# Optimization experiments

Measured on AMD Instinct MI355X. Metric: run time of the kernel, lower is better.

## Reference

```python
import jax, jax.numpy as jnp
import numpy as np

H = 128            # hidden_dim
R = 16             # num_rbf
L = 3              # num_atom_encoder_layers
LAT = 32           # latent_dim
NUM_ATOM_TYPES = 64
CUTOFF = 5.0       # atom_cutoff
N_RES = 2048
DEG = 16           # avg radius-graph degree
_PATTERN = np.array([19, 20, 21, 22, 23, 24, 25, 22])  # ragged atoms/residue, mean 22


def setup_inputs() -> dict:
    key = jax.random.key(0)
    ks = jax.random.split(key, 16)
    apr = np.tile(_PATTERN, N_RES // len(_PATTERN))        # (N,) atoms per residue
    A = int(apr.sum())                                     # 45056 atoms
    E = A * DEG                                            # 720896 edges
    rng = np.random.default_rng(0)

    def gl(k, shape, fan_in):
        return jax.random.normal(k, shape, jnp.float32) * (fan_in ** -0.5)

    return {
        "atom_coords": jax.random.normal(ks[0], (A, 3), jnp.float32) * 10.0,
        "atom_types": jax.random.randint(ks[1], (A,), 0, NUM_ATOM_TYPES),
        "residue_indices": jnp.asarray(np.repeat(np.arange(N_RES), apr)),
        "residue_types": jax.random.randint(ks[2], (N_RES,), 0, 4),
        "atoms_per_residue": jnp.asarray(apr),
        "edge_src": jnp.asarray(rng.integers(0, A, E)),
        "edge_dst": jnp.asarray(rng.integers(0, A, E)),
        # learned parameters
        "atom_embed": gl(ks[3], (NUM_ATOM_TYPES, H), 1.0),
        "residue_embed": gl(ks[4], (4, H), 1.0),
        "We1": gl(ks[5], (L, 2 * H + R, H), 2 * H + R), "be1": jnp.zeros((L, H)),
        "We2": gl(ks[6], (L, H, H), H), "be2": jnp.zeros((L, H)),
        "Wh1": gl(ks[7], (L, 2 * H, H), 2 * H), "bh1": jnp.zeros((L, H)),
        "Wh2": gl(ks[8], (L, H, H), H), "bh2": jnp.zeros((L, H)),
        "Wq": gl(ks[9], (H, H), H), "bq": jnp.zeros((H,)),
        "Wk": gl(ks[10], (H, H), H), "bk": jnp.zeros((H,)),
        "Wv": gl(ks[11], (H, H), H), "bv": jnp.zeros((H,)),
        "Wmu": gl(ks[12], (H, LAT), H), "bmu": jnp.zeros((LAT,)),
        "Wlv": gl(ks[13], (H, LAT), H) * 0.01, "blv": jnp.full((LAT,), -2.0),
    }


def reference(atom_coords, atom_types, residue_indices, residue_types,
              atoms_per_residue, edge_src, edge_dst,
              atom_embed, residue_embed,
              We1, be1, We2, be2, Wh1, bh1, Wh2, bh2,
              Wq, bq, Wk, bk, Wv, bv, Wmu, bmu, Wlv, blv):
    A = atom_coords.shape[0]
    N = residue_types.shape[0]
    coords = atom_coords - atom_coords.mean(0, keepdims=True)  # center_coords

    # Gaussian radial basis expansion of edge distances
    d = jnp.linalg.norm(coords[edge_src] - coords[edge_dst], axis=-1)  # (E,)
    centers = jnp.linspace(0.0, CUTOFF, R)
    gamma = (R / CUTOFF) ** 2
    edge_attr = jnp.exp(-gamma * (d[:, None] - centers) ** 2)          # (E,R)

    # atom features: atom-type embed + residue-type embed scattered to atoms
    res_emb = residue_embed[residue_types]                             # (N,H)
    h = atom_embed[atom_types] + res_emb[residue_indices]              # (A,H)

    # EGNN layers (update_coords=False): message MLP -> sum-agg -> residual node MLP
    for l in range(L):
        m = jnp.concatenate([h[edge_src], h[edge_dst], edge_attr], axis=-1)  # (E,2H+R)
        m = jax.nn.silu(m @ We1[l] + be1[l])
        m = jax.nn.silu(m @ We2[l] + be2[l])                                  # (E,H)
        agg = jax.ops.segment_sum(m, edge_dst, num_segments=A)               # (A,H)
        u = jnp.concatenate([h, agg], axis=-1)                               # (A,2H)
        u = jax.nn.silu(u @ Wh1[l] + bh1[l])
        h = h + (u @ Wh2[l] + bh2[l])

    # segment (per-residue) attention pooling of atoms -> residues
    q = res_emb @ Wq + bq                                              # (N,H)
    k = h @ Wk + bk                                                    # (A,H)
    v = h @ Wv + bv                                                    # (A,H)
    scores = jnp.sum(q[residue_indices] * k, axis=-1) * (H ** -0.5)    # (A,)
    smax = jax.ops.segment_max(scores, residue_indices, num_segments=N)
    ex = jnp.exp(scores - smax[residue_indices])
    denom = jax.ops.segment_sum(ex, residue_indices, num_segments=N)
    w = ex / denom[residue_indices]
    pooled = jax.ops.segment_sum(w[:, None] * v, residue_indices, num_segments=N)  # (N,H)

    mu = pooled @ Wmu + bmu
    logvar = jnp.clip(pooled @ Wlv + blv, -10.0, 2.0)
    return mu, logvar
```

## Files before the change

### kernel.cpp

```cpp
#include <hip/hip_runtime.h>
#include <hip/hip_bf16.h>

#define H 128
#define LATD 32

typedef __attribute__((ext_vector_type(8))) _Float16 half8t;
typedef __attribute__((ext_vector_type(4))) _Float16 half4t;
typedef __attribute__((ext_vector_type(2))) _Float16 half2t;
typedef __attribute__((ext_vector_type(8))) unsigned short u16x8;
typedef __attribute__((ext_vector_type(4))) float f32x4;

#define OFF_RBF 0
#define OFF_W2  12288
#define OFF_PROJ 61440
#define OFF_H1  159744
#define OFF_H2  258048
#define OFF_KV  307200
#define OFF_RBF16 339968
#define WP_TOTAL 346112

__device__ __forceinline__ float silu_f(float x) {
  return x * __builtin_amdgcn_rcpf(1.0f + __expf(-x));
}
__device__ __forceinline__ unsigned short f16u(float x) {
  _Float16 hh = (_Float16)x;
  return *(unsigned short*)&hh;
}

__global__ void k_dist(const float* __restrict__ coords,
                       const int* __restrict__ esrc, const int* __restrict__ edst,
                       float* __restrict__ dbuf, int* __restrict__ cnt, int E) {
  int e = blockIdx.x * blockDim.x + threadIdx.x;
  if (e >= E) return;
  int s = esrc[e], t = edst[e];
  float dx = coords[3*s+0] - coords[3*t+0];
  float dy = coords[3*s+1] - coords[3*t+1];
  float dz = coords[3*s+2] - coords[3*t+2];
  dbuf[e] = sqrtf(dx*dx + dy*dy + dz*dz);
  atomicAdd(&cnt[t], 1);
}

__global__ __launch_bounds__(1024) void k_scanA(const int* __restrict__ cnt,
                                                int* __restrict__ cursor,
                                                int* __restrict__ bsum, int A) {
  __shared__ int buf[1024];
  int tid = threadIdx.x;
  int i = blockIdx.x * 1024 + tid;
  int v = (i < A) ? cnt[i] : 0;
  buf[tid] = v;
  __syncthreads();
  #pragma unroll
  for (int off = 1; off < 1024; off <<= 1) {
    int nv = (tid >= off) ? buf[tid - off] : 0;
    __syncthreads();
    buf[tid] += nv;
    __syncthreads();
  }
  if (i < A) cursor[i] = buf[tid] - v;
  if (tid == 1023) bsum[blockIdx.x] = buf[1023];
}

__global__ void k_scanB(int* __restrict__ bsum, int nb) {
  int lane = threadIdx.x;
  int v = (lane < nb) ? bsum[lane] : 0;
  int s = v;
  #pragma unroll
  for (int off = 1; off < 64; off <<= 1) {
    int nv = __shfl_up(s, off);
    if (lane >= off) s += nv;
  }
  if (lane < nb) bsum[lane] = s - v;
}

__global__ void k_scatter(const int* __restrict__ edst, int* __restrict__ cursor,
                          const int* __restrict__ bsum,
                          int* __restrict__ eperm, int E) {
  int e = blockIdx.x * blockDim.x + threadIdx.x;
  if (e >= E) return;
  int t = edst[e];
  int p = atomicAdd(&cursor[t], 1) + bsum[t >> 10];
  eperm[p] = e;
}

__global__ void k_pack(const float* __restrict__ We1, const float* __restrict__ We2,
                       const float* __restrict__ Wh1, const float* __restrict__ Wh2,
                       const float* __restrict__ Wk,  const float* __restrict__ Wv,
                       unsigned short* __restrict__ wp) {
  int t = blockIdx.x * blockDim.x + threadIdx.x;
  if (t >= WP_TOTAL) return;
  if (t < OFF_W2) {
    wp[t] = 0;
  } else if (t < OFF_PROJ) {
    int u = t - OFF_W2; int layer = u / 16384, idx = u % 16384;
    int i = idx & 7, lane = (idx >> 3) & 63, ct = (idx >> 9) & 7, kt = idx >> 12;
    int k = kt * 32 + (lane >> 4) * 8 + i, c = ct * 16 + (lane & 15);
    const float* src = We2 + (size_t)layer * 128 * H;
    wp[t] = f16u(src[(size_t)k * H + c]);
  } else if (t < OFF_H1) {
    int u = t - OFF_PROJ; int layer = u / 32768, idx = u % 32768;
    int i = idx & 7, lane = (idx >> 3) & 63, ct = (idx >> 9) & 15, kt = idx >> 13;
    int k = kt * 32 + (lane >> 4) * 8 + i, c = ct * 16 + (lane & 15);
    const float* src = We1 + (size_t)layer * 272 * H;
    float v = (c < 128) ? src[(size_t)k * H + c] : src[(size_t)(128 + k) * H + (c - 128)];
    wp[t] = f16u(v);
  } else if (t < OFF_H2) {
    int u = t - OFF_H1; int layer = u / 32768, idx = u % 32768;
    int i = idx & 7, lane = (idx >> 3) & 63, ct = (idx >> 9) & 7, kt = idx >> 12;
    int k = kt * 32 + (lane >> 4) * 8 + i, c = ct * 16 + (lane & 15);
    const float* src = Wh1 + (size_t)layer * 256 * H;
    wp[t] = f16u(src[(size_t)k * H + c]);
  } else if (t < OFF_KV) {
    int u = t - OFF_H2; int layer = u / 16384, idx = u % 16384;
    int i = idx & 7, lane = (idx >> 3) & 63, ct = (idx >> 9) & 7, kt = idx >> 12;
    int k = kt * 32 + (lane >> 4) * 8 + i, c = ct * 16 + (lane & 15);
    const float* src = Wh2 + (size_t)layer * 128 * H;
    wp[t] = f16u(src[(size_t)k * H + c]);
  } else if (t < OFF_RBF16) {
    int idx = t - OFF_KV;
    int i = idx & 7, lane = (idx >> 3) & 63, ct = (idx >> 9) & 15, kt = idx >> 13;
    int k = kt * 32 + (lane >> 4) * 8 + i, c = ct * 16 + (lane & 15);
    float v = (c < 128) ? Wk[(size_t)k * H + c] : Wv[(size_t)k * H + (c - 128)];
    wp[t] = f16u(v);
  } else {
    int u = t - OFF_RBF16; int layer = u / 2048, idx = u % 2048;
    int i = idx & 3, lane = (idx >> 2) & 63, ct = idx >> 8;
    int k = (lane >> 4) * 4 + i;
    int c = ct * 16 + (lane & 15);
    const float* src = We1 + (size_t)layer * 272 * H;
    wp[t] = f16u(src[(size_t)(256 + k) * H + c]);
  }
}

#define PS2 136

__global__ __launch_bounds__(256) void k_init_proj(
    const float* __restrict__ atom_embed, const float* __restrict__ residue_embed,
    const int* __restrict__ atype, const int* __restrict__ ridx,
    const int* __restrict__ rtype,
    float* __restrict__ h, unsigned short* __restrict__ hb,
    int* __restrict__ starts, float* __restrict__ agg,
    const unsigned short* __restrict__ Wp, unsigned short* __restrict__ Ph, int A) {
  __shared__ __align__(16) unsigned short Xp[64 * PS2];
  const int tid = threadIdx.x;
  const int a0 = blockIdx.x * 64;
  {
    const int r = tid >> 2, qt = tid & 3;
    int a = a0 + r;
    int ac = (a < A) ? a : (A - 1);
    int ri = ridx[ac];
    const float* ae = atom_embed + (size_t)atype[ac] * H + qt * 32;
    const float* re = residue_embed + (size_t)rtype[ri] * H + qt * 32;
    if (a < A) {
      if (qt == 0 && (a == 0 || ridx[a - 1] != ri)) starts[ri] = a;
      float4 z = {0.f, 0.f, 0.f, 0.f};
      float4* az = (float4*)(agg + (size_t)a * H + qt * 32);
      #pragma unroll
      for (int i = 0; i < 8; ++i) az[i] = z;
      #pragma unroll
      for (int j = 0; j < 32; ++j) {
        float v = ae[j] + re[j];
        h[(size_t)a * H + qt * 32 + j] = v;
        unsigned short u = f16u(v);
        hb[(size_t)a * H + qt * 32 + j] = u;
        Xp[r * PS2 + qt * 32 + j] = u;
      }
    } else {
      #pragma unroll
      for (int j = 0; j < 32; ++j) {
        float v = ae[j] + re[j];
        Xp[r * PS2 + qt * 32 + j] = f16u(v);
      }
    }
  }
  __syncthreads();
  const int l = tid & 63, wv = tid >> 6;
  const int lr = l & 15, lk = (l >> 4) * 8;
  f32x4 acc[4][4] = {};
  #pragma unroll
  for (int kt = 0; kt < 4; ++kt) {
    half8t a[4], b[4];
    #pragma unroll
    for (int rt = 0; rt < 4; ++rt)
      a[rt] = *(const half8t*)&Xp[(rt * 16 + lr) * PS2 + kt * 32 + lk];
    #pragma unroll
    for (int ci = 0; ci < 4; ++ci)
      b[ci] = *(const half8t*)&Wp[(((size_t)kt * 16 + wv * 4 + ci) * 64 + l) * 8];
    #pragma unroll
    for (int rt = 0; rt < 4; ++rt)
      #pragma unroll
      for (int ci = 0; ci < 4; ++ci)
        acc[rt][ci] = __builtin_amdgcn_mfma_f32_16x16x32_f16(a[rt], b[ci], acc[rt][ci], 0, 0, 0);
  }
  #pragma unroll
  for (int rt = 0; rt < 4; ++rt)
    #pragma unroll
    for (int ci = 0; ci < 4; ++ci) {
      int col = (wv * 4 + ci) * 16 + lr;
      #pragma unroll
      for (int rr = 0; rr < 4; ++rr) {
        int row = a0 + rt * 16 + (l >> 4) * 4 + rr;
        if (row < A) Ph[(size_t)row * 256 + col] = f16u(acc[rt][ci][rr]);
      }
    }
}

#define ES 136

__global__ __launch_bounds__(256) void k_edge_mfma(
    const unsigned short* __restrict__ Ph, const float* __restrict__ dbuf,
    const int* __restrict__ esrc, const int* __restrict__ edst,
    const int* __restrict__ eperm,
    const unsigned short* __restrict__ Wr16, const float* __restrict__ be1,
    const unsigned short* __restrict__ W2p, const float* __restrict__ be2,
    float* __restrict__ agg, int E) {
  __shared__ __align__(16) unsigned short SH[64 * ES];
  __shared__ int dstv[64];
  __shared__ float dval[64];

  const int tid = threadIdx.x;
  const int e0 = blockIdx.x * 64;
  const int l = tid & 63, wv = tid >> 6;
  const int lr = l & 15, lk = (l >> 4) * 8, g4 = (l >> 4) * 4;
  const int ct0 = wv * 2;

  {
    const int r = tid >> 2, qt = tid & 3;
    int e = e0 + r;
    int ec = (e < E) ? e : (E - 1);
    int es = eperm[ec];
    int s = esrc[es], t = edst[es];
    if (qt == 0) {
      dstv[r] = (e < E) ? t : -1;
      dval[r] = dbuf[es];
    }
    const half8t* ps = (const half8t*)(Ph + (size_t)s * 256);
    const half8t* pt = (const half8t*)(Ph + (size_t)t * 256 + 128);
    half8t* pr = (half8t*)&SH[r * ES];
    #pragma unroll
    for (int i = 0; i < 4; ++i)
      pr[qt * 4 + i] = ps[qt * 4 + i] + pt[qt * 4 + i];
  }
  __syncthreads();

  f32x4 acc[2][4];
  #pragma unroll
  for (int cj = 0; cj < 2; ++cj) {
    int cbase = (ct0 + cj) * 16 + g4;
    #pragma unroll
    for (int et = 0; et < 4; ++et) {
      half4t p4 = *(const half4t*)&SH[(et * 16 + lr) * ES + cbase];
      acc[cj][et][0] = (float)p4[0];
      acc[cj][et][1] = (float)p4[1];
      acc[cj][et][2] = (float)p4[2];
      acc[cj][et][3] = (float)p4[3];
    }
  }
  {
    half4t br[4];
    #pragma unroll
    for (int et = 0; et < 4; ++et) {
      float d = dval[et * 16 + lr];
      #pragma unroll
      for (int i = 0; i < 4; ++i) {
        float dd = d - (float)(g4 + i) * (5.0f / 15.0f);
        br[et][i] = (_Float16)__expf(-10.24f * dd * dd);
      }
    }
    half4t ar[2];
    #pragma unroll
    for (int cj = 0; cj < 2; ++cj)
      ar[cj] = *(const half4t*)&Wr16[(((size_t)(ct0 + cj)) * 64 + l) * 4];
    #pragma unroll
    for (int et = 0; et < 4; ++et)
      #pragma unroll
      for (int cj = 0; cj < 2; ++cj)
        acc[cj][et] = __builtin_amdgcn_mfma_f32_16x16x16f16(ar[cj], br[et], acc[cj][et], 0, 0, 0);
  }
  __syncthreads();

  #pragma unroll
  for (int cj = 0; cj < 2; ++cj) {
    f32x4 b1v = *(const f32x4*)&be1[(ct0 + cj) * 16 + g4];
    #pragma unroll
    for (int et = 0; et < 4; ++et) {
      half4t m4;
      #pragma unroll
      for (int rr = 0; rr < 4; ++rr)
        m4[rr] = (_Float16)silu_f(acc[cj][et][rr] + b1v[rr]);
      *(half4t*)&SH[(et * 16 + lr) * ES + (ct0 + cj) * 16 + g4] = m4;
    }
  }
  __syncthreads();

  f32x4 acc2[2][4] = {};
  #pragma unroll
  for (int kt = 0; kt < 4; ++kt) {
    half8t a2[2], b2[4];
    #pragma unroll
    for (int cj = 0; cj < 2; ++cj)
      a2[cj] = *(const half8t*)&W2p[(((size_t)kt * 8 + ct0 + cj) * 64 + l) * 8];
    #pragma unroll
    for (int et = 0; et < 4; ++et)
      b2[et] = *(const half8t*)&SH[(et * 16 + lr) * ES + kt * 32 + lk];
    #pragma unroll
    for (int cj = 0; cj < 2; ++cj)
      #pragma unroll
      for (int et = 0; et < 4; ++et)
        acc2[cj][et] = __builtin_amdgcn_mfma_f32_16x16x32_f16(a2[cj], b2[et], acc2[cj][et], 0, 0, 0);
  }
  __syncthreads();

  #pragma unroll
  for (int cj = 0; cj < 2; ++cj) {
    f32x4 b2v = *(const f32x4*)&be2[(ct0 + cj) * 16 + g4];
    #pragma unroll
    for (int et = 0; et < 4; ++et) {
      half4t m4;
      #pragma unroll
      for (int rr = 0; rr < 4; ++rr)
        m4[rr] = (_Float16)silu_f(acc2[cj][et][rr] + b2v[rr]);
      *(half4t*)&SH[(et * 16 + lr) * ES + (ct0 + cj) * 16 + g4] = m4;
    }
  }
  __syncthreads();

  {
    int cp = tid & 63, qr = tid >> 6;
    int rbeg = qr * 16, rend = rbeg + 16;
    float a0 = 0.f, a1 = 0.f;
    int prev = -1;
    for (int r = rbeg; r < rend; ++r) {
      int dv = dstv[r];
      half2t v = *(const half2t*)&SH[r * ES + cp * 2];
      if (dv != prev) {
        if (prev >= 0) {
          atomicAdd(&agg[(size_t)prev * H + cp * 2], a0);
          atomicAdd(&agg[(size_t)prev * H + cp * 2 + 1], a1);
        }
        a0 = a1 = 0.f;
        prev = dv;
      }
      if (dv >= 0) { a0 += (float)v[0]; a1 += (float)v[1]; }
    }
    if (prev >= 0) {
      atomicAdd(&agg[(size_t)prev * H + cp * 2], a0);
      atomicAdd(&agg[(size_t)prev * H + cp * 2 + 1], a1);
    }
  }
}

#define NXS2 264
#define US2 136

__global__ __launch_bounds__(256) void k_node_proj(
    float* __restrict__ h, unsigned short* __restrict__ hb,
    float* __restrict__ agg, int zero_agg,
    const unsigned short* __restrict__ W1p, const float* __restrict__ bh1,
    const unsigned short* __restrict__ W2p, const float* __restrict__ bh2,
    const unsigned short* __restrict__ Wp, const float* __restrict__ pbias,
    unsigned short* __restrict__ PhOut, int A) {
  __shared__ __align__(16) unsigned short X2[64 * NXS2];
  __shared__ __align__(16) unsigned short Us2[64 * US2];
  const int tid = threadIdx.x;
  const int a0 = blockIdx.x * 64;
  {
    const int r = tid >> 2, qt = tid & 3;
    int a = a0 + r; if (a >= A) a = A - 1;
    const u16x8* hr = (const u16x8*)(hb + (size_t)a * H + qt * 32);
    u16x8* xr = (u16x8*)&X2[r * NXS2 + qt * 32];
    xr[0] = hr[0]; xr[1] = hr[1]; xr[2] = hr[2]; xr[3] = hr[3];
    float4* ar = (float4*)(agg + (size_t)a * H + qt * 32);
    u16x8 tmp[4];
    unsigned short* tp = (unsigned short*)tmp;
    #pragma unroll
    for (int i = 0; i < 8; ++i) {
      float4 av = ar[i];
      tp[i*4+0] = f16u(av.x); tp[i*4+1] = f16u(av.y);
      tp[i*4+2] = f16u(av.z); tp[i*4+3] = f16u(av.w);
    }
    u16x8* xg = (u16x8*)&X2[r * NXS2 + 128 + qt * 32];
    xg[0] = tmp[0]; xg[1] = tmp[1]; xg[2] = tmp[2]; xg[3] = tmp[3];
    if (zero_agg) {
      float4 z = {0.f, 0.f, 0.f, 0.f};
      #pragma unroll
      for (int i = 0; i < 8; ++i) ar[i] = z;
    }
  }
  __syncthreads();

  const int l = tid & 63, wv = tid >> 6;
  const int lr = l & 15, lk = (l >> 4) * 8;
  const int ct0 = wv * 2;

  f32x4 acc[4][2] = {};
  #pragma unroll
  for (int kt = 0; kt < 8; ++kt) {
    half8t a[4], b[2];
    #pragma unroll
    for (int rt = 0; rt < 4; ++rt)
      a[rt] = *(const half8t*)&X2[(rt * 16 + lr) * NXS2 + kt * 32 + lk];
    #pragma unroll
    for (int j = 0; j < 2; ++j)
      b[j] = *(const half8t*)&W1p[(((size_t)kt * 8 + ct0 + j) * 64 + l) * 8];
    #pragma unroll
    for (int rt = 0; rt < 4; ++rt)
      #pragma unroll
      for (int j = 0; j < 2; ++j)
        acc[rt][j] = __builtin_amdgcn_mfma_f32_16x16x32_f16(a[rt], b[j], acc[rt][j], 0, 0, 0);
  }
  #pragma unroll
  for (int rt = 0; rt < 4; ++rt)
    #pragma unroll
    for (int j = 0; j < 2; ++j) {
      int col = (ct0 + j) * 16 + lr;
      float bb = bh1[col];
      #pragma unroll
      for (int rr = 0; rr < 4; ++rr) {
        int row = rt * 16 + (l >> 4) * 4 + rr;
        Us2[row * US2 + col] = f16u(silu_f(acc[rt][j][rr] + bb));
      }
    }
  __syncthreads();

  f32x4 acc2[4][2] = {};
  #pragma unroll
  for (int kt = 0; kt < 4; ++kt) {
    half8t a[4], b[2];
    #pragma unroll
    for (int rt = 0; rt < 4; ++rt)
      a[rt] = *(const half8t*)&Us2[(rt * 16 + lr) * US2 + kt * 32 + lk];
    #pragma unroll
    for (int j = 0; j < 2; ++j)
      b[j] = *(const half8t*)&W2p[(((size_t)kt * 8 + ct0 + j) * 64 + l) * 8];
    #pragma unroll
    for (int rt = 0; rt < 4; ++rt)
      #pragma unroll
      for (int j = 0; j < 2; ++j)
        acc2[rt][j] = __builtin_amdgcn_mfma_f32_16x16x32_f16(a[rt], b[j], acc2[rt][j], 0, 0, 0);
  }
  unsigned short* NH = X2;
  __syncthreads();
  #pragma unroll
  for (int rt = 0; rt < 4; ++rt)
    #pragma unroll
    for (int j = 0; j < 2; ++j) {
      int col = (ct0 + j) * 16 + lr;
      float bb = bh2[col];
      #pragma unroll
      for (int rr = 0; rr < 4; ++rr) {
        int row = rt * 16 + (l >> 4) * 4 + rr;
        int a = a0 + row;
        float nh = 0.0f;
        if (a < A) {
          size_t off = (size_t)a * H + col;
          nh = h[off] + acc2[rt][j][rr] + bb;
          h[off] = nh;
          hb[off] = f16u(nh);
        }
        NH[row * US2 + col] = f16u(nh);
      }
    }
  __syncthreads();

  f32x4 accp[4][4] = {};
  #pragma unroll
  for (int kt = 0; kt < 4; ++kt) {
    half8t a[4], b[4];
    #pragma unroll
    for (int rt = 0; rt < 4; ++rt)
      a[rt] = *(const half8t*)&NH[(rt * 16 + lr) * US2 + kt * 32 + lk];
    #pragma unroll
    for (int ci = 0; ci < 4; ++ci)
      b[ci] = *(const half8t*)&Wp[(((size_t)kt * 16 + wv * 4 + ci) * 64 + l) * 8];
    #pragma unroll
    for (int rt = 0; rt < 4; ++rt)
      #pragma unroll
      for (int ci = 0; ci < 4; ++ci)
        accp[rt][ci] = __builtin_amdgcn_mfma_f32_16x16x32_f16(a[rt], b[ci], accp[rt][ci], 0, 0, 0);
  }
  #pragma unroll
  for (int rt = 0; rt < 4; ++rt)
    #pragma unroll
    for (int ci = 0; ci < 4; ++ci) {
      int col = (wv * 4 + ci) * 16 + lr;
      float bb = pbias ? pbias[col] : 0.0f;
      #pragma unroll
      for (int rr = 0; rr < 4; ++rr) {
        int row = a0 + rt * 16 + (l >> 4) * 4 + rr;
        if (row < A) PhOut[(size_t)row * 256 + col] = f16u(accp[rt][ci][rr] + bb);
      }
    }
}

__global__ void k_q4b(const float* __restrict__ residue_embed,
                      const float* __restrict__ Wq, const float* __restrict__ bq,
                      const float* __restrict__ bk, const float* __restrict__ bv,
                      float* __restrict__ q4, float* __restrict__ bkv) {
  int i = blockIdx.x * blockDim.x + threadIdx.x;
  if (i < 512) {
    int r = i >> 7, j = i & 127;
    const float* emb = residue_embed + (size_t)r * H;
    float s = bq[j];
    #pragma unroll 4
    for (int k = 0; k < H; ++k) s += emb[k] * Wq[(size_t)k*H + j];
    q4[i] = s;
  } else if (i < 768) {
    int t = i - 512;
    bkv[t] = (t < 128) ? bk[t] : bv[t - 128];
  }
}

__global__ void k_score(const unsigned short* __restrict__ kv,
                        const float* __restrict__ q4,
                        const int* __restrict__ ridx,
                        const int* __restrict__ rtype,
                        float* __restrict__ scores, int A) {
  int t = blockIdx.x * blockDim.x + threadIdx.x;
  int a = t >> 2, qt = t & 3;
  if (a >= A) return;
  const half8t* kr = (const half8t*)(kv + (size_t)a * 256 + qt * 32);
  const float* qrow = q4 + (size_t)rtype[ridx[a]] * H + qt * 32;
  float s = 0.f;
  #pragma unroll
  for (int i = 0; i < 4; ++i) {
    half8t kvv = kr[i];
    #pragma unroll
    for (int j = 0; j < 8; ++j) s += (float)kvv[j] * qrow[i * 8 + j];
  }
  s += __shfl_xor(s, 1);
  s += __shfl_xor(s, 2);
  if (qt == 0) scores[a] = s * 0.08838834764831845f;
}

__global__ __launch_bounds__(256) void k_pool(
    const float* __restrict__ scores,
    const unsigned short* __restrict__ kv, const int* __restrict__ starts,
    const int* __restrict__ apr, float* __restrict__ pooled, int N) {
  int r = blockIdx.x * 4 + (threadIdx.x >> 6);
  if (r >= N) return;
  int lane = threadIdx.x & 63;
  int s0 = starts[r], cnt = apr[r];
  float val = (lane < cnt) ? scores[s0 + lane] : -1e30f;
  float mx = val;
  #pragma unroll
  for (int off = 32; off; off >>= 1) mx = fmaxf(mx, __shfl_xor(mx, off));
  float ex = (lane < cnt) ? __expf(val - mx) : 0.0f;
  float sum = ex;
  #pragma unroll
  for (int off = 32; off; off >>= 1) sum += __shfl_xor(sum, off);
  float w = ex * __builtin_amdgcn_rcpf(sum);
  float p0 = 0.f, p1 = 0.f;
  for (int i = 0; i < cnt; ++i) {
    float wi = __shfl(w, i);
    const unsigned short* vr = kv + (size_t)(s0 + i) * 256 + 128;
    p0 += wi * (float)(*(const _Float16*)&vr[lane]);
    p1 += wi * (float)(*(const _Float16*)&vr[64 + lane]);
  }
  pooled[(size_t)r*H + lane] = p0;
  pooled[(size_t)r*H + 64 + lane] = p1;
}

__global__ void k_head(const float* __restrict__ pooled,
                       const float* __restrict__ Wmu, const float* __restrict__ bmu,
                       const float* __restrict__ Wlv, const float* __restrict__ blv,
                       float* __restrict__ out, int N) {
  int i = blockIdx.x * blockDim.x + threadIdx.x;
  if (i >= N * LATD) return;
  int r = i >> 5, j = i & 31;
  const float* p = pooled + (size_t)r * H;
  float smu = 0.f, slv = 0.f;
  #pragma unroll 4
  for (int k = 0; k < H; ++k) {
    float pv = p[k];
    smu += pv * Wmu[(size_t)k*LATD + j];
    slv += pv * Wlv[(size_t)k*LATD + j];
  }
  smu += bmu[j];
  slv += blv[j];
  slv = fminf(fmaxf(slv, -10.0f), 2.0f);
  out[i] = smu;
  out[(size_t)N*LATD + i] = slv;
}

extern "C" void kernel_launch(void* const* d_in, const int* in_sizes, int n_in,
                              void* d_out, int out_size, void* d_ws, size_t ws_size,
                              hipStream_t stream) {
  const float* coords        = (const float*)d_in[0];
  const int*   atype         = (const int*)d_in[1];
  const int*   ridx          = (const int*)d_in[2];
  const int*   rtype         = (const int*)d_in[3];
  const int*   apr           = (const int*)d_in[4];
  const int*   esrc          = (const int*)d_in[5];
  const int*   edst          = (const int*)d_in[6];
  const float* atom_embed    = (const float*)d_in[7];
  const float* residue_embed = (const float*)d_in[8];
  const float* We1 = (const float*)d_in[9];
  const float* be1 = (const float*)d_in[10];
  const float* We2 = (const float*)d_in[11];
  const float* be2 = (const float*)d_in[12];
  const float* Wh1 = (const float*)d_in[13];
  const float* bh1 = (const float*)d_in[14];
  const float* Wh2 = (const float*)d_in[15];
  const float* bh2 = (const float*)d_in[16];
  const float* Wq  = (const float*)d_in[17];
  const float* bq  = (const float*)d_in[18];
  const float* Wk  = (const float*)d_in[19];
  const float* bk  = (const float*)d_in[20];
  const float* Wv  = (const float*)d_in[21];
  const float* bv  = (const float*)d_in[22];
  const float* Wmu = (const float*)d_in[23];
  const float* bmu = (const float*)d_in[24];
  const float* Wlv = (const float*)d_in[25];
  const float* blv = (const float*)d_in[26];

  const int A = in_sizes[1];
  const int N = in_sizes[3];
  const int E = in_sizes[5];

  float* ws     = (float*)d_ws;
  float* h      = ws;
  float* agg    = h + (size_t)A * H;
  float* vbuf   = agg + (size_t)A * H;
  float* dbuf   = vbuf + (size_t)A * H;
  float* q4     = dbuf + (size_t)E;
  float* bkv    = q4 + 4 * H;
  float* pooled = bkv + 256;
  int*   starts = (int*)(pooled + (size_t)N * H);
  unsigned short* hbuf = (unsigned short*)(starts + N);
  int*   eperm  = (int*)(hbuf + (size_t)A * H);
  int*   cnt    = eperm + (size_t)E;
  int*   cursor = cnt + A;
  int*   bsum   = cursor + A;
  unsigned short* wp = (unsigned short*)(bsum + 64);
  unsigned short* Ph = (unsigned short*)vbuf;

  hipMemsetAsync(cnt, 0, (size_t)A * sizeof(int), stream);
  k_pack<<<(WP_TOTAL + 255) / 256, 256, 0, stream>>>(We1, We2, Wh1, Wh2, Wk, Wv, wp);
  k_q4b<<<3, 256, 0, stream>>>(residue_embed, Wq, bq, bk, bv, q4, bkv);
  k_dist<<<(E + 255) / 256, 256, 0, stream>>>(coords, esrc, edst, dbuf, cnt, E);
  k_init_proj<<<(A + 63) / 64, 256, 0, stream>>>(
      atom_embed, residue_embed, atype, ridx, rtype,
      h, hbuf, starts, agg, wp + OFF_PROJ, Ph, A);

  const int nb = (A + 1023) / 1024;
  k_scanA<<<nb, 1024, 0, stream>>>(cnt, cursor, bsum, A);
  k_scanB<<<1, 64, 0, stream>>>(bsum, nb);
  k_scatter<<<(E + 255) / 256, 256, 0, stream>>>(edst, cursor, bsum, eperm, E);

  const int egrid = (E + 63) / 64;
  unsigned short* kv = Ph;
  for (int l = 0; l < 3; ++l) {
    k_edge_mfma<<<egrid, 256, 0, stream>>>(
        Ph, dbuf, esrc, edst, eperm,
        wp + OFF_RBF16 + (size_t)l * 2048, be1 + (size_t)l * H,
        wp + OFF_W2    + (size_t)l * 16384, be2 + (size_t)l * H, agg, E);
    const unsigned short* Wnext =
        (l < 2) ? (wp + OFF_PROJ + (size_t)(l + 1) * 32768) : (wp + OFF_KV);
    k_node_proj<<<(A + 63) / 64, 256, 0, stream>>>(
        h, hbuf, agg, (l < 2) ? 1 : 0,
        wp + OFF_H1 + (size_t)l * 32768, bh1 + (size_t)l * H,
        wp + OFF_H2 + (size_t)l * 16384, bh2 + (size_t)l * H,
        Wnext, (l < 2) ? nullptr : bkv, Ph, A);
  }

  float* scores = dbuf;
  k_score<<<(A * 4 + 255) / 256, 256, 0, stream>>>(kv, q4, ridx, rtype, scores, A);
  k_pool<<<(N + 3) / 4, 256, 0, stream>>>(scores, kv, starts, apr, pooled, N);
  k_head<<<(N * LATD + 255) / 256, 256, 0, stream>>>(pooled, Wmu, bmu, Wlv, blv,
                                                     (float*)d_out, N);
}
```

Baseline: 590.3 us.

## Drop fp32 hidden state, pad coords to float4, MFMA-transpose edge accumulator init

Removes the fp32 copy of the node hidden state, so residual updates now read and write only the fp16 buffer. This cuts global traffic but accumulates rounding error across the three layers. Atom coordinates are padded to float4 in a small pre-pass so each distance gather is a single vector load. In the edge kernel, the per-element fp16-to-fp32 accumulator init is replaced by an identity-matrix MFMA that transposes the projected features into accumulator layout. A launch-bounds occupancy hint of 8 is also added to that kernel.

```diff
diff --git a/kernel.cpp b/kernel.cpp
--- a/kernel.cpp
+++ b/kernel.cpp
@@ -10,7 +10,6 @@
 typedef __attribute__((ext_vector_type(8))) unsigned short u16x8;
 typedef __attribute__((ext_vector_type(4))) float f32x4;
 
-#define OFF_RBF 0
 #define OFF_W2  12288
 #define OFF_PROJ 61440
 #define OFF_H1  159744
@@ -27,15 +26,20 @@
   return *(unsigned short*)&hh;
 }
 
-__global__ void k_dist(const float* __restrict__ coords,
+__global__ void k_pad4(const float* __restrict__ coords, float4* __restrict__ c4, int A) {
+  int a = blockIdx.x * blockDim.x + threadIdx.x;
+  if (a >= A) return;
+  c4[a] = make_float4(coords[3*a], coords[3*a+1], coords[3*a+2], 0.f);
+}
+
+__global__ void k_dist(const float4* __restrict__ c4,
                        const int* __restrict__ esrc, const int* __restrict__ edst,
                        float* __restrict__ dbuf, int* __restrict__ cnt, int E) {
   int e = blockIdx.x * blockDim.x + threadIdx.x;
   if (e >= E) return;
   int s = esrc[e], t = edst[e];
-  float dx = coords[3*s+0] - coords[3*t+0];
-  float dy = coords[3*s+1] - coords[3*t+1];
-  float dz = coords[3*s+2] - coords[3*t+2];
+  float4 a = c4[s], b = c4[t];
+  float dx = a.x - b.x, dy = a.y - b.y, dz = a.z - b.z;
   dbuf[e] = sqrtf(dx*dx + dy*dy + dz*dz);
   atomicAdd(&cnt[t], 1);
 }
@@ -137,7 +141,7 @@
     const float* __restrict__ atom_embed, const float* __restrict__ residue_embed,
     const int* __restrict__ atype, const int* __restrict__ ridx,
     const int* __restrict__ rtype,
-    float* __restrict__ h, unsigned short* __restrict__ hb,
+    unsigned short* __restrict__ hb,
     int* __restrict__ starts, float* __restrict__ agg,
     const unsigned short* __restrict__ Wp, unsigned short* __restrict__ Ph, int A) {
   __shared__ __align__(16) unsigned short Xp[64 * PS2];
@@ -159,17 +163,14 @@
       #pragma unroll
       for (int j = 0; j < 32; ++j) {
         float v = ae[j] + re[j];
-        h[(size_t)a * H + qt * 32 + j] = v;
         unsigned short u = f16u(v);
         hb[(size_t)a * H + qt * 32 + j] = u;
         Xp[r * PS2 + qt * 32 + j] = u;
       }
     } else {
       #pragma unroll
-      for (int j = 0; j < 32; ++j) {
-        float v = ae[j] + re[j];
-        Xp[r * PS2 + qt * 32 + j] = f16u(v);
-      }
+      for (int j = 0; j < 32; ++j)
+        Xp[r * PS2 + qt * 32 + j] = f16u(ae[j] + re[j]);
     }
   }
   __syncthreads();
@@ -206,7 +207,7 @@
 
 #define ES 136
 
-__global__ __launch_bounds__(256) void k_edge_mfma(
+__global__ __launch_bounds__(256, 8) void k_edge_mfma(
     const unsigned short* __restrict__ Ph, const float* __restrict__ dbuf,
     const int* __restrict__ esrc, const int* __restrict__ edst,
     const int* __restrict__ eperm,
@@ -243,16 +244,20 @@
   __syncthreads();
 
   f32x4 acc[2][4];
-  #pragma unroll
-  for (int cj = 0; cj < 2; ++cj) {
-    int cbase = (ct0 + cj) * 16 + g4;
+  {
+    half8t aI[2];
+    #pragma unroll
+    for (int cj = 0; cj < 2; ++cj)
+      #pragma unroll
+      for (int i = 0; i < 8; ++i)
+        aI[cj][i] = (_Float16)((lk + i == cj * 16 + lr) ? 1.0f : 0.0f);
+    const f32x4 z = {0.f, 0.f, 0.f, 0.f};
     #pragma unroll
     for (int et = 0; et < 4; ++et) {
-      half4t p4 = *(const half4t*)&SH[(et * 16 + lr) * ES + cbase];
-      acc[cj][et][0] = (float)p4[0];
-      acc[cj][et][1] = (float)p4[1];
-      acc[cj][et][2] = (float)p4[2];
-      acc[cj][et][3] = (float)p4[3];
+      half8t bP = *(const half8t*)&SH[(et * 16 + lr) * ES + wv * 32 + lk];
+      #pragma unroll
+      for (int cj = 0; cj < 2; ++cj)
+        acc[cj][et] = __builtin_amdgcn_mfma_f32_16x16x32_f16(aI[cj], bP, z, 0, 0, 0);
     }
   }
   {
@@ -353,7 +358,7 @@
 #define US2 136
 
 __global__ __launch_bounds__(256) void k_node_proj(
-    float* __restrict__ h, unsigned short* __restrict__ hb,
+    unsigned short* __restrict__ hb,
     float* __restrict__ agg, int zero_agg,
     const unsigned short* __restrict__ W1p, const float* __restrict__ bh1,
     const unsigned short* __restrict__ W2p, const float* __restrict__ bh2,
@@ -453,8 +458,8 @@
         float nh = 0.0f;
         if (a < A) {
           size_t off = (size_t)a * H + col;
-          nh = h[off] + acc2[rt][j][rr] + bb;
-          h[off] = nh;
+          float oldh = (float)(*(const _Float16*)&hb[off]);
+          nh = oldh + acc2[rt][j][rr] + bb;
           hb[off] = f16u(nh);
         }
         NH[row * US2 + col] = f16u(nh);
@@ -617,9 +622,8 @@
   const int N = in_sizes[3];
   const int E = in_sizes[5];
 
-  float* ws     = (float*)d_ws;
-  float* h      = ws;
-  float* agg    = h + (size_t)A * H;
+  float4* c4    = (float4*)d_ws;
+  float* agg    = (float*)(c4 + A);
   float* vbuf   = agg + (size_t)A * H;
   float* dbuf   = vbuf + (size_t)A * H;
   float* q4     = dbuf + (size_t)E;
@@ -637,10 +641,11 @@
   hipMemsetAsync(cnt, 0, (size_t)A * sizeof(int), stream);
   k_pack<<<(WP_TOTAL + 255) / 256, 256, 0, stream>>>(We1, We2, Wh1, Wh2, Wk, Wv, wp);
   k_q4b<<<3, 256, 0, stream>>>(residue_embed, Wq, bq, bk, bv, q4, bkv);
-  k_dist<<<(E + 255) / 256, 256, 0, stream>>>(coords, esrc, edst, dbuf, cnt, E);
+  k_pad4<<<(A + 255) / 256, 256, 0, stream>>>(coords, c4, A);
+  k_dist<<<(E + 255) / 256, 256, 0, stream>>>(c4, esrc, edst, dbuf, cnt, E);
   k_init_proj<<<(A + 63) / 64, 256, 0, stream>>>(
       atom_embed, residue_embed, atype, ridx, rtype,
-      h, hbuf, starts, agg, wp + OFF_PROJ, Ph, A);
+      hbuf, starts, agg, wp + OFF_PROJ, Ph, A);
 
   const int nb = (A + 1023) / 1024;
   k_scanA<<<nb, 1024, 0, stream>>>(cnt, cursor, bsum, A);
@@ -657,7 +662,7 @@
     const unsigned short* Wnext =
         (l < 2) ? (wp + OFF_PROJ + (size_t)(l + 1) * 32768) : (wp + OFF_KV);
     k_node_proj<<<(A + 63) / 64, 256, 0, stream>>>(
-        h, hbuf, agg, (l < 2) ? 1 : 0,
+        hbuf, agg, (l < 2) ? 1 : 0,
         wp + OFF_H1 + (size_t)l * 32768, bh1 + (size_t)l * H,
         wp + OFF_H2 + (size_t)l * 16384, bh2 + (size_t)l * H,
         Wnext, (l < 2) ? nullptr : bkv, Ph, A);
```

Result: slower. 636.6 us (+7.8%).
